# Kernel optimization log

Measured on AMD Instinct MI355X. Metric: run time of the kernel, lower is better.

Reference implementation:

```python
import jax, jax.numpy as jnp
import numpy as np

C = 256   # descriptor_dim
H = 4     # num_heads
D = C // H  # head_dim = 64
B, N = 8, 2048


def _conv1x1(x, w, b):
    # 1x1 Conv1d == per-position linear over channels: x [B,C,N], w [O,C], b [O]
    return jnp.einsum('oc,bcn->bon', w, x) + b[None, :, None]


def setup_inputs() -> dict:
    key = jax.random.key(0)
    ks = jax.random.split(key, 11)
    s = 1.0 / np.sqrt(C)
    return {
        'query': jax.random.normal(ks[0], (B, C, N), dtype=jnp.float32),
        'key':   jax.random.normal(ks[1], (B, C, N), dtype=jnp.float32),
        'value': jax.random.normal(ks[2], (B, C, N), dtype=jnp.float32),
        'wq': jax.random.normal(ks[3], (C, C), dtype=jnp.float32) * s,
        'bq': jax.random.normal(ks[4], (C,), dtype=jnp.float32) * s,
        'wk': jax.random.normal(ks[5], (C, C), dtype=jnp.float32) * s,
        'bk': jax.random.normal(ks[6], (C,), dtype=jnp.float32) * s,
        'wv': jax.random.normal(ks[7], (C, C), dtype=jnp.float32) * s,
        'bv': jax.random.normal(ks[8], (C,), dtype=jnp.float32) * s,
        'wm': jax.random.normal(ks[9], (C, C), dtype=jnp.float32) * s,
        'bm': jax.random.normal(ks[10], (C,), dtype=jnp.float32) * s,
    }


def reference(query, key, value, wq, bq, wk, bk, wv, bv, wm, bm):
    b = query.shape[0]
    # project then view channels as (head_dim, num_heads) -- matches torch .view order
    q = _conv1x1(query, wq, bq).reshape(b, D, H, -1)   # [B,D,H,N]
    k = _conv1x1(key,   wk, bk).reshape(b, D, H, -1)   # [B,D,H,M]
    v = _conv1x1(value, wv, bv).reshape(b, D, H, -1)   # [B,D,H,M]
    scores = jnp.einsum('bdhn,bdhm->bhnm', q, k) / (D ** 0.5)
    probs = jax.nn.softmax(scores, axis=-1)            # [B,H,N,M]
    out = jnp.einsum('bhnm,bdhm->bdhn', probs, v)      # [B,D,H,N]
    out = out.reshape(b, D * H, -1)                    # [B,C,N]
    return _conv1x1(out, wm, bm)
```

## Files before the change

### kernel.cpp

```cpp
#include <hip/hip_runtime.h>
#include <hip/hip_bf16.h>

typedef float f32x4 __attribute__((ext_vector_type(4)));
typedef float f32x16 __attribute__((ext_vector_type(16)));
typedef __bf16 bf16x8 __attribute__((ext_vector_type(8)));
typedef __bf16 bf16x4 __attribute__((ext_vector_type(4)));
typedef unsigned int uint2v __attribute__((ext_vector_type(2)));

constexpr int B_ = 8, C_ = 256, N_ = 2048, H_ = 4, D_ = 64;
constexpr int BH_ = B_ * H_;
constexpr float LOG2E = 1.44269504088896340736f;

static __device__ __forceinline__ float fast_exp2(float x) {
#if __has_builtin(__builtin_amdgcn_exp2f)
  return __builtin_amdgcn_exp2f(x);
#else
  return exp2f(x);
#endif
}

static __device__ __forceinline__ void* swz(void* base, int row, int cb) {
  return (char*)base + row * 128 + (cb ^ ((row & 7) << 4));
}
static __device__ __forceinline__ const void* swz(const void* base, int row, int cb) {
  return (const char*)base + row * 128 + (cb ^ ((row & 7) << 4));
}

struct W4 {
  const float* s0; const float* s1; const float* s2; const float* s3;
  __bf16* d0; __bf16* d1; __bf16* d2; __bf16* d3;
};

__global__ __launch_bounds__(256) void wcvt_kernel(W4 p) {
  const int m = blockIdx.y;
  const float* src = m == 0 ? p.s0 : m == 1 ? p.s1 : m == 2 ? p.s2 : p.s3;
  __bf16* dst = m == 0 ? p.d0 : m == 1 ? p.d1 : m == 2 ? p.d2 : p.d3;
  const int f = blockIdx.x * 256 + threadIdx.x;
  const int o_blk = f >> 9;
  const int ks = (f >> 6) & 7;
  const int lane = f & 63;
  const int row = o_blk * 16 + (lane & 15);
  const int kbase = ks * 32 + (lane >> 4) * 8;
  bf16x8 v;
  if (m == 3) {
    for (int e = 0; e < 8; e++) {
      const int k = kbase + e;
      const int c = ((k & 63) << 2) | (k >> 6);
      v[e] = (__bf16)src[row * 256 + c];
    }
  } else {
    const int srow = ((row & 63) << 2) | (row >> 6);
    const float* s = src + srow * 256 + kbase;
    float4 a = *(const float4*)s;
    float4 b = *(const float4*)(s + 4);
    v[0] = (__bf16)a.x; v[1] = (__bf16)a.y; v[2] = (__bf16)a.z; v[3] = (__bf16)a.w;
    v[4] = (__bf16)b.x; v[5] = (__bf16)b.y; v[6] = (__bf16)b.z; v[7] = (__bf16)b.w;
  }
  *(bf16x8*)&dst[(size_t)f * 8] = v;
}

__global__ __launch_bounds__(256) void qkv_fused_kernel(
    const float* __restrict__ xq, const float* __restrict__ xk,
    const float* __restrict__ xv, const __bf16* __restrict__ wfq,
    const __bf16* __restrict__ wfk, const __bf16* __restrict__ wfv,
    const float* __restrict__ bq, const float* __restrict__ bk,
    const float* __restrict__ bv, __bf16* __restrict__ oq,
    __bf16* __restrict__ ok, __bf16* __restrict__ ov) {
  __shared__ __bf16 xlds[64][264];

  const int m = blockIdx.x >> 8;
  int inner = blockIdx.x & 255;
  inner = (inner & 7) * 32 + (inner >> 3);
  const int b = inner >> 5, nb = inner & 31;
  const int n0 = nb * 64;

  const float* xf = m == 0 ? xq : m == 1 ? xk : xv;
  const __bf16* wf = m == 0 ? wfq : m == 1 ? wfk : wfv;
  const float* bias = m == 0 ? bq : m == 1 ? bk : bv;
  __bf16* out = m == 0 ? oq : m == 1 ? ok : ov;
  const float scale = m == 0 ? 0.125f * LOG2E : 1.0f;

  const int t = threadIdx.x;
  {
    const int kl = t >> 4;
    const int nl = (t & 15) * 4;
    const float* src = xf + (size_t)b * C_ * N_ + n0 + nl;
    for (int it = 0; it < 16; it++) {
      const int k = it * 16 + kl;
      float4 f = *(const float4*)(src + (size_t)k * N_);
      xlds[nl + 0][k] = (__bf16)f.x;
      xlds[nl + 1][k] = (__bf16)f.y;
      xlds[nl + 2][k] = (__bf16)f.z;
      xlds[nl + 3][k] = (__bf16)f.w;
    }
  }
  __syncthreads();

  const int lane = t & 63, wvv = t >> 6;
  const int wm = wvv >> 1, wn = wvv & 1;
  const int l15 = lane & 15, lg = lane >> 4;

  f32x4 acc[8][2] = {};

  for (int ks = 0; ks < 8; ks++) {
    bf16x8 bfr[2];
    for (int ni = 0; ni < 2; ni++)
      bfr[ni] = *(const bf16x8*)&xlds[wn * 32 + ni * 16 + l15][ks * 32 + lg * 8];
    for (int mi = 0; mi < 8; mi++) {
      bf16x8 af = *(const bf16x8*)&wf[(((size_t)(wm * 8 + mi) * 8 + ks) * 64 + lane) * 8];
      acc[mi][0] = __builtin_amdgcn_mfma_f32_16x16x32_bf16(af, bfr[0], acc[mi][0], 0, 0, 0);
      acc[mi][1] = __builtin_amdgcn_mfma_f32_16x16x32_bf16(af, bfr[1], acc[mi][1], 0, 0, 0);
    }
  }

  for (int mi = 0; mi < 8; mi++) {
    const int h = wm * 2 + (mi >> 2);
    const int d0 = (mi & 3) * 16 + 4 * lg;
    for (int ni = 0; ni < 2; ni++) {
      const int n = n0 + wn * 32 + ni * 16 + l15;
      if (m != 2) {
        bf16x4 o4;
        for (int r = 0; r < 4; r++)
          o4[r] = (__bf16)((acc[mi][ni][r] + bias[((d0 + r) << 2) | h]) * scale);
        *(bf16x4*)&out[((size_t)(b * H_ + h) * N_ + n) * D_ + d0] = o4;
      } else {
        for (int r = 0; r < 4; r++)
          out[((size_t)(b * H_ + h) * D_ + d0 + r) * N_ + n] =
              (__bf16)(acc[mi][ni][r] + bias[((d0 + r) << 2) | h]);
      }
    }
  }
}

__global__ __launch_bounds__(256) void final_proj_kernel(
    const __bf16* __restrict__ xb, const __bf16* __restrict__ wf,
    const float* __restrict__ bias, float* __restrict__ out) {
  const int bid = blockIdx.x;
  const int wid = (bid & 7) * 128 + (bid >> 3);
  const int o_t = wid & 3;
  const int nb = (wid >> 2) & 31;
  const int b = wid >> 7;
  const int o0 = o_t * 64, n0 = nb * 64;
  const int t = threadIdx.x, lane = t & 63;
  const int wvv = t >> 6, wm = wvv >> 1, wn = wvv & 1;
  const int l15 = lane & 15, lg = lane >> 4;
  const int nbase = n0 + wn * 32 + l15;

  f32x4 acc[2][2] = {};

  for (int ks = 0; ks < 8; ks++) {
    bf16x8 af[2];
    for (int mi = 0; mi < 2; mi++)
      af[mi] = *(const bf16x8*)&wf[(((size_t)(o_t * 4 + wm * 2 + mi) * 8 + ks) * 64 + lane) * 8];
    bf16x8 bfr[2];
    const size_t bh = (size_t)(b * H_ + (ks >> 1));
    const int d0 = (ks & 1) * 32 + lg * 8;
    for (int ni = 0; ni < 2; ni++)
      bfr[ni] = *(const bf16x8*)&xb[(bh * N_ + nbase + ni * 16) * D_ + d0];
    for (int mi = 0; mi < 2; mi++)
      for (int ni = 0; ni < 2; ni++)
        acc[mi][ni] = __builtin_amdgcn_mfma_f32_16x16x32_bf16(
            af[mi], bfr[ni], acc[mi][ni], 0, 0, 0);
  }

  for (int mi = 0; mi < 2; mi++) {
    for (int r = 0; r < 4; r++) {
      const int och = o0 + wm * 32 + mi * 16 + 4 * lg + r;
      const float bv_ = bias[och];
      for (int ni = 0; ni < 2; ni++) {
        const int n = n0 + wn * 32 + ni * 16 + l15;
        out[((size_t)b * C_ + och) * N_ + n] = acc[mi][ni][r] + bv_;
      }
    }
  }
}

__global__ __launch_bounds__(256) void attn_kernel(
    const __bf16* __restrict__ qb, const __bf16* __restrict__ kb,
    const __bf16* __restrict__ vtb, __bf16* __restrict__ attout) {
  __shared__ __bf16 kbuf[2][64][64];
  __shared__ __bf16 vtbuf[2][64][64];

  const int t = threadIdx.x, lane = t & 63, wv = t >> 6;
  const int l31 = lane & 31, hi = lane >> 5;

  const int bid = blockIdx.x;
  const int wid = (bid & 7) * 64 + (bid >> 3);
  const int bh = wid >> 4;
  const int qn = (wid & 15) * 128 + wv * 32;

  const __bf16* k_bh = kb + (size_t)bh * N_ * D_;
  const __bf16* vt_bh = vtb + (size_t)bh * D_ * N_;

  const __bf16* qrow = qb + ((size_t)bh * N_ + qn + l31) * D_;
  bf16x8 qf[4];
#pragma unroll
  for (int i = 0; i < 4; i++) qf[i] = *(const bf16x8*)(qrow + i * 16 + hi * 8);

  const int srow = t >> 2, sce = (t & 3) * 16;

  {
    uint4 ka = *(const uint4*)(k_bh + (size_t)srow * D_ + sce);
    uint4 kc = *(const uint4*)(k_bh + (size_t)srow * D_ + sce + 8);
    uint4 va = *(const uint4*)(vt_bh + (size_t)srow * N_ + sce);
    uint4 vc = *(const uint4*)(vt_bh + (size_t)srow * N_ + sce + 8);
    *(uint4*)swz(&kbuf[0][0][0], srow, sce * 2) = ka;
    *(uint4*)swz(&kbuf[0][0][0], srow, sce * 2 + 16) = kc;
    *(uint4*)swz(&vtbuf[0][0][0], srow, sce * 2) = va;
    *(uint4*)swz(&vtbuf[0][0][0], srow, sce * 2 + 16) = vc;
  }
  __syncthreads();

  f32x16 o0 = {}, o1 = {};
  float la0 = 0.f, la1 = 0.f, la2 = 0.f, la3 = 0.f;
  int cur = 0;

  for (int j0 = 0; j0 < N_; j0 += 64) {
    const int jn = j0 + 64;
    const bool have = jn < N_;
    uint4 pka, pkc, pva, pvc;
    if (have) {
      pka = *(const uint4*)(k_bh + (size_t)(jn + srow) * D_ + sce);
      pkc = *(const uint4*)(k_bh + (size_t)(jn + srow) * D_ + sce + 8);
      pva = *(const uint4*)(vt_bh + (size_t)srow * N_ + jn + sce);
      pvc = *(const uint4*)(vt_bh + (size_t)srow * N_ + jn + sce + 8);
    }

    f32x16 s0 = {}, s1 = {};
    __builtin_amdgcn_s_setprio(1);
#pragma unroll
    for (int i = 0; i < 4; i++) {
      bf16x8 kf = *(const bf16x8*)swz(&kbuf[cur][0][0], l31, i * 32 + hi * 16);
      s0 = __builtin_amdgcn_mfma_f32_32x32x16_bf16(kf, qf[i], s0, 0, 0, 0);
    }
#pragma unroll
    for (int i = 0; i < 4; i++) {
      bf16x8 kf = *(const bf16x8*)swz(&kbuf[cur][0][0], 32 + l31, i * 32 + hi * 16);
      s1 = __builtin_amdgcn_mfma_f32_32x32x16_bf16(kf, qf[i], s1, 0, 0, 0);
    }
    __builtin_amdgcn_s_setprio(0);

#pragma unroll
    for (int sub = 0; sub < 2; sub++) {
      const f32x16 s = sub ? s1 : s0;
      float pr[16];
#pragma unroll
      for (int r = 0; r < 16; r++) pr[r] = fast_exp2(s[r]);
      la0 += pr[0] + pr[4] + pr[8] + pr[12];
      la1 += pr[1] + pr[5] + pr[9] + pr[13];
      la2 += pr[2] + pr[6] + pr[10] + pr[14];
      la3 += pr[3] + pr[7] + pr[11] + pr[15];
      unsigned w[8];
#pragma unroll
      for (int g = 0; g < 8; g++) {
        union { __bf16 h[2]; unsigned u; } cv;
        cv.h[0] = (__bf16)pr[2 * g];
        cv.h[1] = (__bf16)pr[2 * g + 1];
        w[g] = cv.u;
      }
      uint2v r0 = __builtin_amdgcn_permlane32_swap(w[0], w[2], false, false);
      uint2v r1 = __builtin_amdgcn_permlane32_swap(w[1], w[3], false, false);
      uint2v r2 = __builtin_amdgcn_permlane32_swap(w[4], w[6], false, false);
      uint2v r3 = __builtin_amdgcn_permlane32_swap(w[5], w[7], false, false);
      union { unsigned u[4]; bf16x8 v; } f0 = {{r0.x, r1.x, r0.y, r1.y}};
      union { unsigned u[4]; bf16x8 v; } f1 = {{r2.x, r3.x, r2.y, r3.y}};
      const int scb = sub * 64;
      __builtin_amdgcn_s_setprio(1);
      {
        bf16x8 vf = *(const bf16x8*)swz(&vtbuf[cur][0][0], l31, scb + hi * 16);
        o0 = __builtin_amdgcn_mfma_f32_32x32x16_bf16(vf, f0.v, o0, 0, 0, 0);
        vf = *(const bf16x8*)swz(&vtbuf[cur][0][0], l31, scb + 32 + hi * 16);
        o0 = __builtin_amdgcn_mfma_f32_32x32x16_bf16(vf, f1.v, o0, 0, 0, 0);
        vf = *(const bf16x8*)swz(&vtbuf[cur][0][0], 32 + l31, scb + hi * 16);
        o1 = __builtin_amdgcn_mfma_f32_32x32x16_bf16(vf, f0.v, o1, 0, 0, 0);
        vf = *(const bf16x8*)swz(&vtbuf[cur][0][0], 32 + l31, scb + 32 + hi * 16);
        o1 = __builtin_amdgcn_mfma_f32_32x32x16_bf16(vf, f1.v, o1, 0, 0, 0);
      }
      __builtin_amdgcn_s_setprio(0);
    }

    if (have) {
      const int nxt = cur ^ 1;
      *(uint4*)swz(&kbuf[nxt][0][0], srow, sce * 2) = pka;
      *(uint4*)swz(&kbuf[nxt][0][0], srow, sce * 2 + 16) = pkc;
      *(uint4*)swz(&vtbuf[nxt][0][0], srow, sce * 2) = pva;
      *(uint4*)swz(&vtbuf[nxt][0][0], srow, sce * 2 + 16) = pvc;
      __syncthreads();
    }
    cur ^= 1;
  }

  float la = la0 + la1 + la2 + la3;
  la += __shfl_xor(la, 32);
  const float inv = 1.f / la;

  __syncthreads();
  char* ep = (char*)&vtbuf[0][0][0] + wv * 4096;
#pragma unroll
  for (int dt = 0; dt < 2; dt++) {
    const f32x16 o = dt ? o1 : o0;
#pragma unroll
    for (int g = 0; g < 4; g++) {
      bf16x4 o4;
#pragma unroll
      for (int j = 0; j < 4; j++) o4[j] = (__bf16)(o[4 * g + j] * inv);
      *(bf16x4*)swz(ep, l31, dt * 64 + 16 * g + 8 * hi) = o4;
    }
  }
  asm volatile("" ::: "memory");
  {
    __bf16* dst = attout + ((size_t)bh * N_ + qn) * D_;
#pragma unroll
    for (int i = 0; i < 4; i++) {
      const int row = i * 8 + (lane >> 3);
      uint4 v = *(const uint4*)swz(ep, row, (lane & 7) * 16);
      *(uint4*)((char*)dst + i * 1024 + lane * 16) = v;
    }
  }
}

extern "C" void kernel_launch(void* const* d_in, const int* in_sizes, int n_in,
                              void* d_out, int out_size, void* d_ws,
                              size_t ws_size, hipStream_t stream) {
  const float* query = (const float*)d_in[0];
  const float* key_ = (const float*)d_in[1];
  const float* value = (const float*)d_in[2];
  const float* wq = (const float*)d_in[3];
  const float* bq = (const float*)d_in[4];
  const float* wk = (const float*)d_in[5];
  const float* bk = (const float*)d_in[6];
  const float* wv = (const float*)d_in[7];
  const float* bv = (const float*)d_in[8];
  const float* wm = (const float*)d_in[9];
  const float* bm = (const float*)d_in[10];

  const size_t per = (size_t)BH_ * N_ * D_;
  __bf16* qb = (__bf16*)d_ws;
  __bf16* kb = qb + per;
  __bf16* vtb = kb + per;
  __bf16* attout = vtb + per;
  __bf16* wfq = attout + per;
  __bf16* wfk = wfq + 65536;
  __bf16* wfv = wfk + 65536;
  __bf16* wfm = wfv + 65536;

  dim3 blk(256);
  W4 wp{wq, wk, wv, wm, wfq, wfk, wfv, wfm};
  wcvt_kernel<<<dim3(32, 4), blk, 0, stream>>>(wp);

  qkv_fused_kernel<<<768, blk, 0, stream>>>(query, key_, value, wfq, wfk, wfv,
                                            bq, bk, bv, qb, kb, vtb);
  attn_kernel<<<512, blk, 0, stream>>>(qb, kb, vtb, attout);
  final_proj_kernel<<<1024, blk, 0, stream>>>(attout, wfm, bm, (float*)d_out);
}
```

Measured before the change: 105.2 us.

## Split attention KV range across two blocks and combine partial outputs

Result: slower. 107.5 us (+2.2%).

```diff
diff --git a/kernel.cpp b/kernel.cpp
--- a/kernel.cpp
+++ b/kernel.cpp
@@ -9,6 +9,7 @@
 
 constexpr int B_ = 8, C_ = 256, N_ = 2048, H_ = 4, D_ = 64;
 constexpr int BH_ = B_ * H_;
+constexpr size_t PER_ = (size_t)BH_ * N_ * D_;
 constexpr float LOG2E = 1.44269504088896340736f;
 
 static __device__ __forceinline__ float fast_exp2(float x) {
@@ -175,9 +176,11 @@
   }
 }
 
+template <int SPLIT>
 __global__ __launch_bounds__(256) void attn_kernel(
     const __bf16* __restrict__ qb, const __bf16* __restrict__ kb,
-    const __bf16* __restrict__ vtb, __bf16* __restrict__ attout) {
+    const __bf16* __restrict__ vtb, __bf16* __restrict__ pO,
+    float* __restrict__ lbuf) {
   __shared__ __bf16 kbuf[2][64][64];
   __shared__ __bf16 vtbuf[2][64][64];
 
@@ -185,9 +188,13 @@
   const int l31 = lane & 31, hi = lane >> 5;
 
   const int bid = blockIdx.x;
-  const int wid = (bid & 7) * 64 + (bid >> 3);
+  const int s = (SPLIT > 1) ? (bid >> 9) : 0;
+  const int inner = bid & 511;
+  const int wid = (inner & 7) * 64 + (inner >> 3);
   const int bh = wid >> 4;
   const int qn = (wid & 15) * 128 + wv * 32;
+  const int jbase = s * (N_ / SPLIT);
+  constexpr int NT = N_ / SPLIT / 64;
 
   const __bf16* k_bh = kb + (size_t)bh * N_ * D_;
   const __bf16* vt_bh = vtb + (size_t)bh * D_ * N_;
@@ -200,10 +207,10 @@
   const int srow = t >> 2, sce = (t & 3) * 16;
 
   {
-    uint4 ka = *(const uint4*)(k_bh + (size_t)srow * D_ + sce);
-    uint4 kc = *(const uint4*)(k_bh + (size_t)srow * D_ + sce + 8);
-    uint4 va = *(const uint4*)(vt_bh + (size_t)srow * N_ + sce);
-    uint4 vc = *(const uint4*)(vt_bh + (size_t)srow * N_ + sce + 8);
+    uint4 ka = *(const uint4*)(k_bh + (size_t)(jbase + srow) * D_ + sce);
+    uint4 kc = *(const uint4*)(k_bh + (size_t)(jbase + srow) * D_ + sce + 8);
+    uint4 va = *(const uint4*)(vt_bh + (size_t)srow * N_ + jbase + sce);
+    uint4 vc = *(const uint4*)(vt_bh + (size_t)srow * N_ + jbase + sce + 8);
     *(uint4*)swz(&kbuf[0][0][0], srow, sce * 2) = ka;
     *(uint4*)swz(&kbuf[0][0][0], srow, sce * 2 + 16) = kc;
     *(uint4*)swz(&vtbuf[0][0][0], srow, sce * 2) = va;
@@ -215,11 +222,12 @@
   float la0 = 0.f, la1 = 0.f, la2 = 0.f, la3 = 0.f;
   int cur = 0;
 
-  for (int j0 = 0; j0 < N_; j0 += 64) {
-    const int jn = j0 + 64;
-    const bool have = jn < N_;
+  for (int jt = 0; jt < NT; jt++) {
+    const int j0 = jbase + jt * 64;
+    const bool have = (jt + 1) < NT;
     uint4 pka, pkc, pva, pvc;
     if (have) {
+      const int jn = j0 + 64;
       pka = *(const uint4*)(k_bh + (size_t)(jn + srow) * D_ + sce);
       pkc = *(const uint4*)(k_bh + (size_t)(jn + srow) * D_ + sce + 8);
       pva = *(const uint4*)(vt_bh + (size_t)srow * N_ + jn + sce);
@@ -242,10 +250,10 @@
 
 #pragma unroll
     for (int sub = 0; sub < 2; sub++) {
-      const f32x16 s = sub ? s1 : s0;
+      const f32x16 sv = sub ? s1 : s0;
       float pr[16];
 #pragma unroll
-      for (int r = 0; r < 16; r++) pr[r] = fast_exp2(s[r]);
+      for (int r = 0; r < 16; r++) pr[r] = fast_exp2(sv[r]);
       la0 += pr[0] + pr[4] + pr[8] + pr[12];
       la1 += pr[1] + pr[5] + pr[9] + pr[13];
       la2 += pr[2] + pr[6] + pr[10] + pr[14];
@@ -292,7 +300,12 @@
 
   float la = la0 + la1 + la2 + la3;
   la += __shfl_xor(la, 32);
-  const float inv = 1.f / la;
+  const float scl = (SPLIT == 1) ? 1.f / la : 1.f;
+
+  if constexpr (SPLIT > 1) {
+    if (hi == 0)
+      lbuf[(size_t)s * BH_ * N_ + (size_t)bh * N_ + qn + l31] = la;
+  }
 
   __syncthreads();
   char* ep = (char*)&vtbuf[0][0][0] + wv * 4096;
@@ -303,13 +316,13 @@
     for (int g = 0; g < 4; g++) {
       bf16x4 o4;
 #pragma unroll
-      for (int j = 0; j < 4; j++) o4[j] = (__bf16)(o[4 * g + j] * inv);
+      for (int j = 0; j < 4; j++) o4[j] = (__bf16)(o[4 * g + j] * scl);
       *(bf16x4*)swz(ep, l31, dt * 64 + 16 * g + 8 * hi) = o4;
     }
   }
   asm volatile("" ::: "memory");
   {
-    __bf16* dst = attout + ((size_t)bh * N_ + qn) * D_;
+    __bf16* dst = pO + (size_t)s * PER_ + ((size_t)bh * N_ + qn) * D_;
 #pragma unroll
     for (int i = 0; i < 4; i++) {
       const int row = i * 8 + (lane >> 3);
@@ -317,6 +330,21 @@
       *(uint4*)((char*)dst + i * 1024 + lane * 16) = v;
     }
   }
+}
+
+__global__ __launch_bounds__(256) void combine_kernel(
+    const __bf16* __restrict__ p0, const __bf16* __restrict__ p1,
+    const float* __restrict__ l0, const float* __restrict__ l1,
+    __bf16* __restrict__ outp) {
+  const size_t idx8 = (size_t)blockIdx.x * 256 + threadIdx.x;
+  const size_t nidx = idx8 >> 3;
+  bf16x8 a = *(const bf16x8*)&p0[idx8 * 8];
+  bf16x8 b = *(const bf16x8*)&p1[idx8 * 8];
+  const float inv = 1.f / (l0[nidx] + l1[nidx]);
+  bf16x8 r;
+#pragma unroll
+  for (int e = 0; e < 8; e++) r[e] = (__bf16)(((float)a[e] + (float)b[e]) * inv);
+  *(bf16x8*)&outp[idx8 * 8] = r;
 }
 
 extern "C" void kernel_launch(void* const* d_in, const int* in_sizes, int n_in,
@@ -334,22 +362,35 @@
   const float* wm = (const float*)d_in[9];
   const float* bm = (const float*)d_in[10];
 
-  const size_t per = (size_t)BH_ * N_ * D_;
   __bf16* qb = (__bf16*)d_ws;
-  __bf16* kb = qb + per;
-  __bf16* vtb = kb + per;
-  __bf16* attout = vtb + per;
-  __bf16* wfq = attout + per;
+  __bf16* kb = qb + PER_;
+  __bf16* vtb = kb + PER_;
+  __bf16* p0 = vtb + PER_;
+  __bf16* p1 = p0 + PER_;
+  float* lbuf = (float*)(p1 + PER_);
+  __bf16* wfq = (__bf16*)(lbuf + 2 * BH_ * N_);
   __bf16* wfk = wfq + 65536;
   __bf16* wfv = wfk + 65536;
   __bf16* wfm = wfv + 65536;
 
+  const size_t need_split = (size_t)((char*)(wfm + 65536) - (char*)d_ws);
+  const bool use_split = ws_size >= need_split;
+
   dim3 blk(256);
   W4 wp{wq, wk, wv, wm, wfq, wfk, wfv, wfm};
+  if (!use_split) {
+    wfq = p1; wfk = wfq + 65536; wfv = wfk + 65536; wfm = wfv + 65536;
+    wp = W4{wq, wk, wv, wm, wfq, wfk, wfv, wfm};
+  }
   wcvt_kernel<<<dim3(32, 4), blk, 0, stream>>>(wp);
 
   qkv_fused_kernel<<<768, blk, 0, stream>>>(query, key_, value, wfq, wfk, wfv,
                                             bq, bk, bv, qb, kb, vtb);
-  attn_kernel<<<512, blk, 0, stream>>>(qb, kb, vtb, attout);
-  final_proj_kernel<<<1024, blk, 0, stream>>>(attout, wfm, bm, (float*)d_out);
-}
+  if (use_split) {
+    attn_kernel<2><<<1024, blk, 0, stream>>>(qb, kb, vtb, p0, lbuf);
+    combine_kernel<<<2048, blk, 0, stream>>>(p0, p1, lbuf, lbuf + BH_ * N_, p0);
+  } else {
+    attn_kernel<1><<<512, blk, 0, stream>>>(qb, kb, vtb, p0, nullptr);
+  }
+  final_proj_kernel<<<1024, blk, 0, stream>>>(p0, wfm, bm, (float*)d_out);
+}
```
